# Optimization experiments

Measured on AMD Instinct MI355X. Metric: run time of the kernel, lower is better.

## Reference

```python
import jax, jax.numpy as jnp
import numpy as np
from jax import lax

B, N, C = 8, 8192, 91          # batch, num_boxes, num_classes (incl. background)
CM = C - 1                      # foreground classes
K = 1000                        # pre_nms_num_detections (per-class candidates / max per class)
MAX_TOTAL = 100                 # post_nms_num_detections
IOU_THR = 0.3
SCORE_THR = 0.0
BBOX_W = (10.0, 10.0, 5.0, 5.0)
BBOX_CLIP = float(np.log(1000.0 / 16.0))
IMG = 1024.0


def setup_inputs() -> dict:
    key = jax.random.key(0)
    k1, k2, k3, k4, k5, k6 = jax.random.split(key, 6)
    class_outputs = jax.random.normal(k1, (B, N, C), jnp.float32)
    box_outputs = jax.random.normal(k2, (B, N, C * 4), jnp.float32)
    cy = jax.random.uniform(k3, (B, N), minval=0.0, maxval=IMG)
    cx = jax.random.uniform(k4, (B, N), minval=0.0, maxval=IMG)
    sh = jax.random.uniform(k5, (B, N), minval=16.0, maxval=256.0)
    sw = jax.random.uniform(k6, (B, N), minval=16.0, maxval=256.0)
    anchor_boxes = jnp.stack([
        jnp.clip(cy - 0.5 * sh, 0.0, IMG), jnp.clip(cx - 0.5 * sw, 0.0, IMG),
        jnp.clip(cy + 0.5 * sh, 0.0, IMG), jnp.clip(cx + 0.5 * sw, 0.0, IMG)], axis=-1)
    image_info = jnp.tile(jnp.array([IMG, IMG, 1.0, 1.0], jnp.float32), (B, 1))
    return {"class_outputs": class_outputs, "box_outputs": box_outputs,
            "anchor_boxes": anchor_boxes, "image_info": image_info}


def decode_boxes(enc, anchors):
    # enc, anchors: [..., 4] (ty,tx,th,tw) / (ymin,xmin,ymax,xmax)
    wy, wx, wh, ww = BBOX_W
    ah = anchors[..., 2] - anchors[..., 0]
    aw = anchors[..., 3] - anchors[..., 1]
    acy = anchors[..., 0] + 0.5 * ah
    acx = anchors[..., 1] + 0.5 * aw
    ty = enc[..., 0] / wy
    tx = enc[..., 1] / wx
    th = jnp.minimum(enc[..., 2] / wh, BBOX_CLIP)
    tw = jnp.minimum(enc[..., 3] / ww, BBOX_CLIP)
    cy = ty * ah + acy
    cx = tx * aw + acx
    h = jnp.exp(th) * ah
    w = jnp.exp(tw) * aw
    return jnp.stack([cy - 0.5 * h, cx - 0.5 * w, cy + 0.5 * h, cx + 0.5 * w], axis=-1)


def pairwise_iou(b):  # b: [K,4] -> [K,K]
    area = jnp.maximum(b[:, 2] - b[:, 0], 0.0) * jnp.maximum(b[:, 3] - b[:, 1], 0.0)
    ih = jnp.maximum(jnp.minimum(b[:, None, 2], b[None, :, 2]) - jnp.maximum(b[:, None, 0], b[None, :, 0]), 0.0)
    iw = jnp.maximum(jnp.minimum(b[:, None, 3], b[None, :, 3]) - jnp.maximum(b[:, None, 1], b[None, :, 1]), 0.0)
    inter = ih * iw
    return inter / (area[:, None] + area[None, :] - inter + 1e-8)


def _per_class_nms(bc, sc):
    # bc: [N,4] normalized boxes, sc: [N] scores -> (kept boxes [K,4], scores [K], suppressed -> -1)
    sk, idx = lax.top_k(sc, K)
    bk = bc[idx]
    overlap = pairwise_iou(bk) > IOU_THR   # bool [K,K], sorted by score desc
    pass_thr = sk > SCORE_THR
    def body(i, keep):
        sup = jnp.any(keep & overlap[:, i])
        return keep.at[i].set(pass_thr[i] & jnp.logical_not(sup))
    keep = lax.fori_loop(0, K, body, jnp.zeros((K,), jnp.bool_))
    return bk, jnp.where(keep, sk, -1.0)


def _per_image(norm_boxes, sc):
    # norm_boxes: [N,CM,4], sc: [N,CM]
    bks, sks = jax.vmap(_per_class_nms)(jnp.transpose(norm_boxes, (1, 0, 2)), sc.T)
    fs = sks.reshape(-1)          # [CM*K]
    fb = bks.reshape(-1, 4)
    ts, ti = lax.top_k(fs, MAX_TOTAL)
    tb = fb[ti]
    tc = (ti // K).astype(jnp.float32)   # 0-based fg class index
    valid = ts > SCORE_THR
    ts = jnp.where(valid, ts, 0.0)
    tb = jnp.where(valid[:, None], tb, 0.0)
    tc = jnp.where(valid, tc, 0.0)
    return tb, ts, tc, jnp.sum(valid).astype(jnp.int32)


def reference(class_outputs, box_outputs, anchor_boxes, image_info):
    probs = jax.nn.softmax(class_outputs, axis=-1)
    scores = probs[..., 1:]                                   # [B,N,CM]
    enc = box_outputs.reshape(B, N, C, 4)[:, :, 1:, :]        # [B,N,CM,4]
    anchors = jnp.broadcast_to(anchor_boxes[:, :, None, :], (B, N, CM, 4))
    boxes = decode_boxes(enc, anchors)                        # [B,N,CM,4]
    h = image_info[:, 0]
    w = image_info[:, 1]
    hw = jnp.stack([h, w, h, w], axis=-1)                     # [B,4]
    boxes = jnp.clip(boxes, 0.0, hw[:, None, None, :])        # clip to image
    norm_boxes = boxes / hw[:, None, None, :]                 # to_normalized_coordinates
    pb, ps, pc, nv = lax.map(lambda a: _per_image(*a), (norm_boxes, scores))
    post_boxes = pb * hw[:, None, :]                          # to_absolute_coordinates
    post_classes = pc + 1.0                                   # shift back over background
    return (nv, post_boxes, post_classes, ps)
```

## Files before the change

### kernel.cpp

```cpp
#include <hip/hip_runtime.h>
#include <math.h>

#define Bb 8
#define Nn 8192
#define Cc 91
#define CM 90
#define Kk 1000
#define MAXT 100
#define KSEL 256
#define NW 4
#define IOU_THR 0.3f
#define BBOX_CLIP 4.135166556742356f
#define IMG 1024.0f
#define SM_ROWS 64

typedef unsigned long long u64;
typedef unsigned int u32;

__global__ __launch_bounds__(64) void softmax_scores(
    const float* __restrict__ cls, float* __restrict__ scores_t) {
    __shared__ float rowbuf[SM_ROWS * Cc];
    int blk = blockIdx.x;
    int lane = threadIdx.x;
    const float4* src = (const float4*)(cls + (size_t)blk * SM_ROWS * Cc);
    for (int i = lane; i < SM_ROWS * Cc / 4; i += 64) {
        float4 v = src[i];
        *(float4*)&rowbuf[i * 4] = v;
    }
    __syncthreads();
    int row_g = blk * SM_ROWS + lane;
    int b = row_g >> 13;
    int n = row_g & (Nn - 1);
    const float* row = &rowbuf[lane * Cc];
    float m = row[0];
    for (int c = 1; c < Cc; c++) m = fmaxf(m, row[c]);
    float s = 0.0f;
    for (int c = 0; c < Cc; c++) s += expf(row[c] - m);
    for (int c = 1; c < Cc; c++) {
        float p = expf(row[c] - m) / s;
        scores_t[((size_t)(b * CM + (c - 1))) * Nn + n] = p;
    }
}

__global__ __launch_bounds__(512) void topk_nms(
    const float* __restrict__ scores_t,
    const float* __restrict__ box_out, const float* __restrict__ anchors,
    u64* __restrict__ cand_key, float* __restrict__ cand_box) {
    __shared__ __align__(16) char smem[36896];
    u32* sbits = (u32*)smem;
    int* hist  = (int*)(smem + 32768);
    int* scal  = (int*)(smem + 36864);
    u64* keys  = (u64*)(smem + 32768);
    int* eqidx = (int*)(smem + 34816);
    u64* keys2 = (u64*)(smem);
    float* dy1 = (float*)(smem + 2048);
    float* dx1 = (float*)(smem + 3072);
    float* dy2 = (float*)(smem + 4096);
    float* dx2 = (float*)(smem + 5120);
    float* dar = (float*)(smem + 6144);
    float4* kb = (float4*)(smem + 7168);
    float* kar = (float*)(smem + 8768);
    u64* kkey  = (u64*)(smem + 9168);
    #define sh_need  scal[0]
    #define sh_digit scal[1]
    #define sh_cnt   scal[2]
    #define sh_eq    scal[3]
    #define sh_kcnt  scal[4]

    int bc = blockIdx.x;
    int b = bc / CM;
    int c = bc % CM;
    int tid = threadIdx.x;
    int wave = tid >> 6, lane = tid & 63;

    hist[tid] = 0;
    hist[tid + 512] = 0;
    if (tid == 0) { sh_need = KSEL; sh_cnt = 0; sh_eq = 0; }
    __syncthreads();

    const float4* s4 = (const float4*)(scores_t + (size_t)bc * Nn);
    float4 v0 = s4[tid];
    float4 v1 = s4[tid + 512];
    float4 v2 = s4[tid + 1024];
    float4 v3 = s4[tid + 1536];
    u32 x[16];
    x[0]  = __float_as_uint(v0.x); x[1]  = __float_as_uint(v0.y);
    x[2]  = __float_as_uint(v0.z); x[3]  = __float_as_uint(v0.w);
    x[4]  = __float_as_uint(v1.x); x[5]  = __float_as_uint(v1.y);
    x[6]  = __float_as_uint(v1.z); x[7]  = __float_as_uint(v1.w);
    x[8]  = __float_as_uint(v2.x); x[9]  = __float_as_uint(v2.y);
    x[10] = __float_as_uint(v2.z); x[11] = __float_as_uint(v2.w);
    x[12] = __float_as_uint(v3.x); x[13] = __float_as_uint(v3.y);
    x[14] = __float_as_uint(v3.z); x[15] = __float_as_uint(v3.w);
    *(uint4*)&sbits[(tid)        * 4] = make_uint4(x[0], x[1], x[2], x[3]);
    *(uint4*)&sbits[(tid + 512)  * 4] = make_uint4(x[4], x[5], x[6], x[7]);
    *(uint4*)&sbits[(tid + 1024) * 4] = make_uint4(x[8], x[9], x[10], x[11]);
    *(uint4*)&sbits[(tid + 1536) * 4] = make_uint4(x[12], x[13], x[14], x[15]);
    #pragma unroll
    for (int k = 0; k < 16; k++) atomicAdd(&hist[x[k] >> 20], 1);
    __syncthreads();

    #define SELECT_DIGIT()                                                   \
    if (wave == 0) {                                                         \
        int4 h0 = *(const int4*)&hist[16 * lane];                            \
        int4 h1 = *(const int4*)&hist[16 * lane + 4];                        \
        int4 h2 = *(const int4*)&hist[16 * lane + 8];                        \
        int4 h3 = *(const int4*)&hist[16 * lane + 12];                       \
        int cnt[16] = {h0.x, h0.y, h0.z, h0.w, h1.x, h1.y, h1.z, h1.w,       \
                       h2.x, h2.y, h2.z, h2.w, h3.x, h3.y, h3.z, h3.w};      \
        int gsum = 0;                                                        \
        _Pragma("unroll")                                                    \
        for (int j = 0; j < 16; j++) gsum += cnt[j];                         \
        int run = gsum;                                                      \
        for (int off = 1; off < 64; off <<= 1) {                             \
            int vv = __shfl_down(run, off, 64);                              \
            if (lane + off < 64) run += vv;                                  \
        }                                                                    \
        int sa = run - gsum;                                                 \
        int need = sh_need;                                                  \
        if (need > sa && need <= sa + gsum) {                                \
            int acc = sa;                                                    \
            _Pragma("unroll")                                                \
            for (int j = 15; j >= 0; j--) {                                  \
                if (acc + cnt[j] >= need) {                                  \
                    sh_digit = 16 * lane + j;                                \
                    sh_need = need - acc;                                    \
                    break;                                                   \
                }                                                            \
                acc += cnt[j];                                               \
            }                                                                \
        }                                                                    \
    }

    SELECT_DIGIT();
    __syncthreads();
    u32 P12 = (u32)sh_digit;

    hist[tid] = 0;
    hist[tid + 512] = 0;
    __syncthreads();
    for (int i = tid; i < Nn / 4; i += 512) {
        uint4 v = *(const uint4*)&sbits[i * 4];
        if ((v.x >> 20) == P12) atomicAdd(&hist[(v.x >> 10) & 1023], 1);
        if ((v.y >> 20) == P12) atomicAdd(&hist[(v.y >> 10) & 1023], 1);
        if ((v.z >> 20) == P12) atomicAdd(&hist[(v.z >> 10) & 1023], 1);
        if ((v.w >> 20) == P12) atomicAdd(&hist[(v.w >> 10) & 1023], 1);
    }
    __syncthreads();
    SELECT_DIGIT();
    __syncthreads();
    u32 P22 = (P12 << 10) | (u32)sh_digit;

    hist[tid] = 0;
    hist[tid + 512] = 0;
    __syncthreads();
    for (int i = tid; i < Nn / 4; i += 512) {
        uint4 v = *(const uint4*)&sbits[i * 4];
        if ((v.x >> 10) == P22) atomicAdd(&hist[v.x & 1023], 1);
        if ((v.y >> 10) == P22) atomicAdd(&hist[v.y & 1023], 1);
        if ((v.z >> 10) == P22) atomicAdd(&hist[v.z & 1023], 1);
        if ((v.w >> 10) == P22) atomicAdd(&hist[v.w & 1023], 1);
    }
    __syncthreads();
    SELECT_DIGIT();
    __syncthreads();
    u32 Tb = (P22 << 10) | (u32)sh_digit;
    int m = sh_need;
    #undef SELECT_DIGIT

    for (int i = tid; i < Nn / 4; i += 512) {
        uint4 v4 = *(const uint4*)&sbits[i * 4];
        u32 vs[4] = {v4.x, v4.y, v4.z, v4.w};
        #pragma unroll
        for (int k = 0; k < 4; k++) {
            u32 v = vs[k];
            int idx = i * 4 + k;
            if (v > Tb) {
                int pp = atomicAdd(&sh_cnt, 1);
                keys[pp] = ((u64)v << 13) | (u64)(8191 - idx);
            } else if (v == Tb) {
                int pp = atomicAdd(&sh_eq, 1);
                if (pp < 256) eqidx[pp] = idx;
            }
        }
    }
    __syncthreads();
    if (tid == 0) {
        int e = min(sh_eq, 256);
        for (int t = 0; t < m; t++) {
            int best = -1, bi = 0x7FFFFFFF;
            for (int q = 0; q < e; q++) {
                int ii = eqidx[q];
                if (ii < bi) { bi = ii; best = q; }
            }
            if (best >= 0) {
                eqidx[best] = 0x7FFFFFFF;
                int pp = atomicAdd(&sh_cnt, 1);
                keys[pp] = ((u64)Tb << 13) | (u64)(8191 - bi);
            }
        }
    }
    __syncthreads();

    if (tid < KSEL) {
        u64 my = keys[tid];
        int n = 8191 - (int)(my & 0x1FFF);
        const float4 e = *(const float4*)(box_out + ((size_t)(b * Nn + n)) * (Cc * 4) + (size_t)(c + 1) * 4);
        const float4 a = *(const float4*)(anchors + (size_t)(b * Nn + n) * 4);
        int r = 0;
        #pragma unroll 8
        for (int q = 0; q < KSEL; q++) r += (keys[q] > my) ? 1 : 0;
        keys2[r] = my;
        float ah = a.z - a.x, aw = a.w - a.y;
        float acy = a.x + 0.5f * ah, acx = a.y + 0.5f * aw;
        float ty = e.x / 10.0f, tx = e.y / 10.0f;
        float th = fminf(e.z / 5.0f, BBOX_CLIP);
        float tw = fminf(e.w / 5.0f, BBOX_CLIP);
        float cy = ty * ah + acy, cx = tx * aw + acx;
        float h = expf(th) * ah, w = expf(tw) * aw;
        float y1 = cy - 0.5f * h, x1 = cx - 0.5f * w;
        float y2 = cy + 0.5f * h, x2 = cx + 0.5f * w;
        y1 = fminf(fmaxf(y1, 0.0f), IMG) * (1.0f / IMG);
        x1 = fminf(fmaxf(x1, 0.0f), IMG) * (1.0f / IMG);
        y2 = fminf(fmaxf(y2, 0.0f), IMG) * (1.0f / IMG);
        x2 = fminf(fmaxf(x2, 0.0f), IMG) * (1.0f / IMG);
        float area = fmaxf(y2 - y1, 0.0f) * fmaxf(x2 - x1, 0.0f);
        dy1[r] = y1; dx1[r] = x1;
        dy2[r] = y2; dx2[r] = x2;
        dar[r] = area;
    }
    __syncthreads();

    if (tid < 64) {
        int kcnt = 0;
        for (int ci = 0; ci < NW && kcnt < MAXT; ci++) {
            int i = ci * 64 + lane;
            u64 key = keys2[i];
            float sc = __uint_as_float((u32)(key >> 13));
            float y1 = dy1[i], x1 = dx1[i];
            float y2 = dy2[i], x2 = dx2[i];
            float area = dar[i];

            bool sup = false;
            for (int r = 0; r < kcnt; r++) {
                float4 kv = kb[r];
                float ka = kar[r];
                float ih = fmaxf(fminf(kv.z, y2) - fmaxf(kv.x, y1), 0.0f);
                float iw = fmaxf(fminf(kv.w, x2) - fmaxf(kv.y, x1), 0.0f);
                float inter = ih * iw;
                sup = sup | (inter > IOU_THR * (ka + area - inter + 1e-8f));
            }
            u64 rem = __ballot((sc > 0.0f) && !sup);
            while (rem != 0ull && kcnt < MAXT) {
                int j = __ffsll(rem) - 1;
                rem &= rem - 1;
                float jy1 = __shfl(y1, j), jx1 = __shfl(x1, j);
                float jy2 = __shfl(y2, j), jx2 = __shfl(x2, j);
                float jar = __shfl(area, j);
                if (lane == j) {
                    kb[kcnt] = make_float4(y1, x1, y2, x2);
                    kar[kcnt] = area;
                    int flat = c * Kk + i;
                    kkey[kcnt] = ((u64)__float_as_uint(sc) << 32)
                               | ((u64)(u32)(131071 - flat) << 14)
                               | (u64)(u32)(c * MAXT + kcnt);
                }
                float ih = fmaxf(fminf(jy2, y2) - fmaxf(jy1, y1), 0.0f);
                float iw = fmaxf(fminf(jx2, x2) - fmaxf(jx1, x1), 0.0f);
                float inter = ih * iw;
                bool ov = inter > IOU_THR * (jar + area - inter + 1e-8f);
                u64 mm = __ballot(ov);
                rem &= ~mm;
                kcnt++;
            }
        }
        if (lane == 0) sh_kcnt = kcnt;
    }
    __syncthreads();

    int kcnt = sh_kcnt;
    for (int r = tid; r < MAXT; r += 512) {
        int slot = bc * MAXT + r;
        if (r < kcnt) {
            cand_key[slot] = kkey[r];
            float4 v = kb[r];
            cand_box[slot * 4 + 0] = v.x;
            cand_box[slot * 4 + 1] = v.y;
            cand_box[slot * 4 + 2] = v.z;
            cand_box[slot * 4 + 3] = v.w;
        } else {
            cand_key[slot] = 0ull;
        }
    }
    #undef sh_need
    #undef sh_digit
    #undef sh_cnt
    #undef sh_eq
    #undef sh_kcnt
}

__global__ __launch_bounds__(256) void final_topk(
    const u64* __restrict__ cand_key, const float* __restrict__ cand_box,
    float* __restrict__ out) {
    extern __shared__ u64 sk[];
    __shared__ u64 res[MAXT];
    int b = blockIdx.x;
    int tid = threadIdx.x;

    for (int i = tid; i < CM * MAXT; i += 256)
        sk[i] = cand_key[b * CM * MAXT + i];
    __syncthreads();

    if (tid < 64) {
        int lane = tid;
        int c0 = lane, c1 = lane + 64;
        bool h1 = c1 < CM;
        int p0 = 0, p1 = 0;
        u64 k0 = sk[c0 * MAXT + 0];
        u64 k0n = sk[c0 * MAXT + 1];
        u64 k1 = h1 ? sk[c1 * MAXT + 0] : 0ull;
        u64 k1n = h1 ? sk[c1 * MAXT + 1] : 0ull;
        for (int t = 0; t < MAXT; t++) {
            u64 m = (k0 > k1) ? k0 : k1;
            for (int off = 32; off > 0; off >>= 1) {
                u64 o = __shfl_xor(m, off);
                if (o > m) m = o;
            }
            if (lane == 0) res[t] = m;
            if (m != 0ull) {
                if (m == k0) {
                    p0++; k0 = k0n;
                    k0n = (p0 + 1 < MAXT) ? sk[c0 * MAXT + p0 + 1] : 0ull;
                } else if (h1 && m == k1) {
                    p1++; k1 = k1n;
                    k1n = (p1 + 1 < MAXT) ? sk[c1 * MAXT + p1 + 1] : 0ull;
                }
            }
        }
    }
    __syncthreads();

    for (int t = tid; t < MAXT; t += 256) {
        u64 m = res[t];
        float sc = __uint_as_float((u32)(m >> 32));
        bool valid = sc > 0.0f;
        float b0 = 0.f, b1 = 0.f, b2 = 0.f, b3 = 0.f, clsv = 0.f, sv = 0.f;
        if (valid) {
            int idx = (int)(m & 0x3FFF);
            int slot = b * CM * MAXT + idx;
            b0 = cand_box[slot * 4 + 0] * IMG;
            b1 = cand_box[slot * 4 + 1] * IMG;
            b2 = cand_box[slot * 4 + 2] * IMG;
            b3 = cand_box[slot * 4 + 3] * IMG;
            clsv = (float)(idx / MAXT + 1);
            sv = sc;
        }
        int o = (b * MAXT + t);
        out[8 + o * 4 + 0] = b0;
        out[8 + o * 4 + 1] = b1;
        out[8 + o * 4 + 2] = b2;
        out[8 + o * 4 + 3] = b3;
        out[8 + Bb * MAXT * 4 + o] = clsv;
        out[8 + Bb * MAXT * 5 + o] = sv;
    }
    if (tid == 0) {
        int nv = 0;
        for (int t = 0; t < MAXT; t++) nv += ((res[t] >> 32) != 0ull) ? 1 : 0;
        out[b] = (float)nv;
    }
}

extern "C" void kernel_launch(void* const* d_in, const int* in_sizes, int n_in,
                              void* d_out, int out_size, void* d_ws, size_t ws_size,
                              hipStream_t stream) {
    (void)in_sizes; (void)n_in; (void)out_size; (void)ws_size;
    const float* cls  = (const float*)d_in[0];
    const float* boxo = (const float*)d_in[1];
    const float* anch = (const float*)d_in[2];
    float* out = (float*)d_out;
    char* ws = (char*)d_ws;

    float* scores_t = (float*)(ws);
    u64*   cand_key = (u64*)  (ws + 23592960);
    float* cand_box = (float*)(ws + 24168960);

    softmax_scores<<<(Bb * Nn) / SM_ROWS, 64, 0, stream>>>(cls, scores_t);
    topk_nms<<<Bb * CM, 512, 0, stream>>>(scores_t, boxo, anch, cand_key, cand_box);
    final_topk<<<Bb, 256, CM * MAXT * sizeof(u64), stream>>>(cand_key, cand_box, out);
}
```

Baseline: 252.5 us.

## Split top-k selection and NMS into separate kernels; cache softmax exponentials

The fused top-k plus NMS kernel is split in two. A 512-thread selection kernel writes the 256 selected keys per class to workspace, and a 256-thread NMS/decode kernel with smaller shared memory reads them back. The aim is to let each phase run at a block size and occupancy suited to it, instead of holding 512 threads through the mostly serial NMS. The softmax kernel also stores each exponential in shared memory so expf is not computed twice. The cost is an extra kernel launch and a global round trip for the keys.

```diff
diff --git a/kernel.cpp b/kernel.cpp
--- a/kernel.cpp
+++ b/kernel.cpp
@@ -31,45 +31,36 @@
     int row_g = blk * SM_ROWS + lane;
     int b = row_g >> 13;
     int n = row_g & (Nn - 1);
-    const float* row = &rowbuf[lane * Cc];
+    float* row = &rowbuf[lane * Cc];
     float m = row[0];
     for (int c = 1; c < Cc; c++) m = fmaxf(m, row[c]);
     float s = 0.0f;
-    for (int c = 0; c < Cc; c++) s += expf(row[c] - m);
+    for (int c = 0; c < Cc; c++) {
+        float e = expf(row[c] - m);
+        row[c] = e;
+        s += e;
+    }
     for (int c = 1; c < Cc; c++) {
-        float p = expf(row[c] - m) / s;
+        float p = row[c] / s;
         scores_t[((size_t)(b * CM + (c - 1))) * Nn + n] = p;
     }
 }
 
-__global__ __launch_bounds__(512) void topk_nms(
+__global__ __launch_bounds__(512) void topk_select(
     const float* __restrict__ scores_t,
-    const float* __restrict__ box_out, const float* __restrict__ anchors,
-    u64* __restrict__ cand_key, float* __restrict__ cand_box) {
+    u64* __restrict__ keys_out) {
     __shared__ __align__(16) char smem[36896];
     u32* sbits = (u32*)smem;
     int* hist  = (int*)(smem + 32768);
     int* scal  = (int*)(smem + 36864);
     u64* keys  = (u64*)(smem + 32768);
     int* eqidx = (int*)(smem + 34816);
-    u64* keys2 = (u64*)(smem);
-    float* dy1 = (float*)(smem + 2048);
-    float* dx1 = (float*)(smem + 3072);
-    float* dy2 = (float*)(smem + 4096);
-    float* dx2 = (float*)(smem + 5120);
-    float* dar = (float*)(smem + 6144);
-    float4* kb = (float4*)(smem + 7168);
-    float* kar = (float*)(smem + 8768);
-    u64* kkey  = (u64*)(smem + 9168);
     #define sh_need  scal[0]
     #define sh_digit scal[1]
     #define sh_cnt   scal[2]
     #define sh_eq    scal[3]
-    #define sh_kcnt  scal[4]
 
     int bc = blockIdx.x;
-    int b = bc / CM;
-    int c = bc % CM;
     int tid = threadIdx.x;
     int wave = tid >> 6, lane = tid & 63;
 
@@ -202,6 +193,40 @@
     }
     __syncthreads();
 
+    if (tid < KSEL) keys_out[(size_t)bc * KSEL + tid] = keys[tid];
+    #undef sh_need
+    #undef sh_digit
+    #undef sh_cnt
+    #undef sh_eq
+}
+
+__global__ __launch_bounds__(256) void nms_decode(
+    const u64* __restrict__ keys_in,
+    const float* __restrict__ box_out, const float* __restrict__ anchors,
+    u64* __restrict__ cand_key, float* __restrict__ cand_box) {
+    __shared__ __align__(16) char smem[12928];
+    u64* keys  = (u64*)smem;
+    u64* keys2 = (u64*)(smem + 2048);
+    float* dy1 = (float*)(smem + 4096);
+    float* dx1 = (float*)(smem + 5120);
+    float* dy2 = (float*)(smem + 6144);
+    float* dx2 = (float*)(smem + 7168);
+    float* dar = (float*)(smem + 8192);
+    float4* kb = (float4*)(smem + 9216);
+    float* kar = (float*)(smem + 10816);
+    u64* kkey  = (u64*)(smem + 11216);
+    int* scal  = (int*)(smem + 12016);
+    #define sh_kcnt scal[0]
+
+    int bc = blockIdx.x;
+    int b = bc / CM;
+    int c = bc % CM;
+    int tid = threadIdx.x;
+    int lane = tid & 63;
+
+    if (tid < KSEL) keys[tid] = keys_in[(size_t)bc * KSEL + tid];
+    __syncthreads();
+
     if (tid < KSEL) {
         u64 my = keys[tid];
         int n = 8191 - (int)(my & 0x1FFF);
@@ -279,7 +304,7 @@
     __syncthreads();
 
     int kcnt = sh_kcnt;
-    for (int r = tid; r < MAXT; r += 512) {
+    for (int r = tid; r < MAXT; r += 256) {
         int slot = bc * MAXT + r;
         if (r < kcnt) {
             cand_key[slot] = kkey[r];
@@ -292,10 +317,6 @@
             cand_key[slot] = 0ull;
         }
     }
-    #undef sh_need
-    #undef sh_digit
-    #undef sh_cnt
-    #undef sh_eq
     #undef sh_kcnt
 }
 
@@ -383,8 +404,10 @@
     float* scores_t = (float*)(ws);
     u64*   cand_key = (u64*)  (ws + 23592960);
     float* cand_box = (float*)(ws + 24168960);
+    u64*   keys_ws  = (u64*)  (ws + 25320960);
 
     softmax_scores<<<(Bb * Nn) / SM_ROWS, 64, 0, stream>>>(cls, scores_t);
-    topk_nms<<<Bb * CM, 512, 0, stream>>>(scores_t, boxo, anch, cand_key, cand_box);
+    topk_select<<<Bb * CM, 512, 0, stream>>>(scores_t, keys_ws);
+    nms_decode<<<Bb * CM, 256, 0, stream>>>(keys_ws, boxo, anch, cand_key, cand_box);
     final_topk<<<Bb, 256, CM * MAXT * sizeof(u64), stream>>>(cand_key, cand_box, out);
 }
```

Result: no change. 253.7 us (+0.5%).

## Keep scores in registers for radix select; double-buffer histograms; cache softmax exps

Applied to the files above, without the earlier changes.

The top-k radix select no longer stages the 8192 scores in shared memory. Each thread keeps its 16 values in registers and re-scans them for every histogram pass and for the final compaction. Two histogram buffers alternate so one can be cleared while wave 0 selects a digit from the other, which removes separate clear-and-sync phases. Shared memory shrinks from about 36KB to 21KB, which may raise occupancy. Softmax also stores exp values in the shared row buffer instead of recomputing expf in the output loop.

```diff
diff --git a/kernel.cpp b/kernel.cpp
--- a/kernel.cpp
+++ b/kernel.cpp
@@ -31,13 +31,17 @@
     int row_g = blk * SM_ROWS + lane;
     int b = row_g >> 13;
     int n = row_g & (Nn - 1);
-    const float* row = &rowbuf[lane * Cc];
+    float* row = &rowbuf[lane * Cc];
     float m = row[0];
     for (int c = 1; c < Cc; c++) m = fmaxf(m, row[c]);
     float s = 0.0f;
-    for (int c = 0; c < Cc; c++) s += expf(row[c] - m);
+    for (int c = 0; c < Cc; c++) {
+        float e = expf(row[c] - m);
+        row[c] = e;
+        s += e;
+    }
     for (int c = 1; c < Cc; c++) {
-        float p = expf(row[c] - m) / s;
+        float p = row[c] / s;
         scores_t[((size_t)(b * CM + (c - 1))) * Nn + n] = p;
     }
 }
@@ -46,21 +50,21 @@
     const float* __restrict__ scores_t,
     const float* __restrict__ box_out, const float* __restrict__ anchors,
     u64* __restrict__ cand_key, float* __restrict__ cand_box) {
-    __shared__ __align__(16) char smem[36896];
-    u32* sbits = (u32*)smem;
-    int* hist  = (int*)(smem + 32768);
-    int* scal  = (int*)(smem + 36864);
-    u64* keys  = (u64*)(smem + 32768);
-    int* eqidx = (int*)(smem + 34816);
-    u64* keys2 = (u64*)(smem);
-    float* dy1 = (float*)(smem + 2048);
-    float* dx1 = (float*)(smem + 3072);
-    float* dy2 = (float*)(smem + 4096);
-    float* dx2 = (float*)(smem + 5120);
-    float* dar = (float*)(smem + 6144);
-    float4* kb = (float4*)(smem + 7168);
-    float* kar = (float*)(smem + 8768);
-    u64* kkey  = (u64*)(smem + 9168);
+    __shared__ __align__(16) char smem[21264];
+    int* hist1 = (int*)smem;
+    int* hist2 = (int*)(smem + 4096);
+    u64* keys  = (u64*)(smem + 8192);
+    int* eqidx = (int*)(smem + 10240);
+    u64* keys2 = (u64*)(smem + 11264);
+    float* dy1 = (float*)(smem + 13312);
+    float* dx1 = (float*)(smem + 14336);
+    float* dy2 = (float*)(smem + 15360);
+    float* dx2 = (float*)(smem + 16384);
+    float* dar = (float*)(smem + 17408);
+    float4* kb = (float4*)(smem + 18432);
+    float* kar = (float*)(smem + 20032);
+    u64* kkey  = (u64*)(smem + 20432);
+    int* scal  = (int*)(smem + 21232);
     #define sh_need  scal[0]
     #define sh_digit scal[1]
     #define sh_cnt   scal[2]
@@ -73,8 +77,8 @@
     int tid = threadIdx.x;
     int wave = tid >> 6, lane = tid & 63;
 
-    hist[tid] = 0;
-    hist[tid + 512] = 0;
+    hist1[tid] = 0; hist1[tid + 512] = 0;
+    hist2[tid] = 0; hist2[tid + 512] = 0;
     if (tid == 0) { sh_need = KSEL; sh_cnt = 0; sh_eq = 0; }
     __syncthreads();
 
@@ -92,20 +96,16 @@
     x[10] = __float_as_uint(v2.z); x[11] = __float_as_uint(v2.w);
     x[12] = __float_as_uint(v3.x); x[13] = __float_as_uint(v3.y);
     x[14] = __float_as_uint(v3.z); x[15] = __float_as_uint(v3.w);
-    *(uint4*)&sbits[(tid)        * 4] = make_uint4(x[0], x[1], x[2], x[3]);
-    *(uint4*)&sbits[(tid + 512)  * 4] = make_uint4(x[4], x[5], x[6], x[7]);
-    *(uint4*)&sbits[(tid + 1024) * 4] = make_uint4(x[8], x[9], x[10], x[11]);
-    *(uint4*)&sbits[(tid + 1536) * 4] = make_uint4(x[12], x[13], x[14], x[15]);
     #pragma unroll
-    for (int k = 0; k < 16; k++) atomicAdd(&hist[x[k] >> 20], 1);
-    __syncthreads();
-
-    #define SELECT_DIGIT()                                                   \
-    if (wave == 0) {                                                         \
-        int4 h0 = *(const int4*)&hist[16 * lane];                            \
-        int4 h1 = *(const int4*)&hist[16 * lane + 4];                        \
-        int4 h2 = *(const int4*)&hist[16 * lane + 8];                        \
-        int4 h3 = *(const int4*)&hist[16 * lane + 12];                       \
+    for (int k = 0; k < 16; k++) atomicAdd(&hist1[x[k] >> 20], 1);
+    __syncthreads();
+
+    #define SELECT_DIGIT(H)                                                  \
+    {                                                                        \
+        int4 h0 = *(const int4*)&(H)[16 * lane];                             \
+        int4 h1 = *(const int4*)&(H)[16 * lane + 4];                         \
+        int4 h2 = *(const int4*)&(H)[16 * lane + 8];                         \
+        int4 h3 = *(const int4*)&(H)[16 * lane + 12];                        \
         int cnt[16] = {h0.x, h0.y, h0.z, h0.w, h1.x, h1.y, h1.z, h1.w,       \
                        h2.x, h2.y, h2.z, h2.w, h3.x, h3.y, h3.z, h3.w};      \
         int gsum = 0;                                                        \
@@ -132,56 +132,41 @@
         }                                                                    \
     }
 
-    SELECT_DIGIT();
+    if (wave == 0) SELECT_DIGIT(hist1);
     __syncthreads();
     u32 P12 = (u32)sh_digit;
 
-    hist[tid] = 0;
-    hist[tid + 512] = 0;
-    __syncthreads();
-    for (int i = tid; i < Nn / 4; i += 512) {
-        uint4 v = *(const uint4*)&sbits[i * 4];
-        if ((v.x >> 20) == P12) atomicAdd(&hist[(v.x >> 10) & 1023], 1);
-        if ((v.y >> 20) == P12) atomicAdd(&hist[(v.y >> 10) & 1023], 1);
-        if ((v.z >> 20) == P12) atomicAdd(&hist[(v.z >> 10) & 1023], 1);
-        if ((v.w >> 20) == P12) atomicAdd(&hist[(v.w >> 10) & 1023], 1);
-    }
-    __syncthreads();
-    SELECT_DIGIT();
+    #pragma unroll
+    for (int k = 0; k < 16; k++)
+        if ((x[k] >> 20) == P12) atomicAdd(&hist2[(x[k] >> 10) & 1023], 1);
+    __syncthreads();
+
+    if (wave == 0) { SELECT_DIGIT(hist2); }
+    else { for (int i = tid - 64; i < 1024; i += 448) hist1[i] = 0; }
     __syncthreads();
     u32 P22 = (P12 << 10) | (u32)sh_digit;
 
-    hist[tid] = 0;
-    hist[tid + 512] = 0;
-    __syncthreads();
-    for (int i = tid; i < Nn / 4; i += 512) {
-        uint4 v = *(const uint4*)&sbits[i * 4];
-        if ((v.x >> 10) == P22) atomicAdd(&hist[v.x & 1023], 1);
-        if ((v.y >> 10) == P22) atomicAdd(&hist[v.y & 1023], 1);
-        if ((v.z >> 10) == P22) atomicAdd(&hist[v.z & 1023], 1);
-        if ((v.w >> 10) == P22) atomicAdd(&hist[v.w & 1023], 1);
-    }
-    __syncthreads();
-    SELECT_DIGIT();
+    #pragma unroll
+    for (int k = 0; k < 16; k++)
+        if ((x[k] >> 10) == P22) atomicAdd(&hist1[x[k] & 1023], 1);
+    __syncthreads();
+
+    if (wave == 0) SELECT_DIGIT(hist1);
     __syncthreads();
     u32 Tb = (P22 << 10) | (u32)sh_digit;
     int m = sh_need;
     #undef SELECT_DIGIT
 
-    for (int i = tid; i < Nn / 4; i += 512) {
-        uint4 v4 = *(const uint4*)&sbits[i * 4];
-        u32 vs[4] = {v4.x, v4.y, v4.z, v4.w};
-        #pragma unroll
-        for (int k = 0; k < 4; k++) {
-            u32 v = vs[k];
-            int idx = i * 4 + k;
-            if (v > Tb) {
-                int pp = atomicAdd(&sh_cnt, 1);
-                keys[pp] = ((u64)v << 13) | (u64)(8191 - idx);
-            } else if (v == Tb) {
-                int pp = atomicAdd(&sh_eq, 1);
-                if (pp < 256) eqidx[pp] = idx;
-            }
+    #pragma unroll
+    for (int k = 0; k < 16; k++) {
+        u32 v = x[k];
+        int idx = ((k >> 2) << 11) + (tid << 2) + (k & 3);
+        if (v > Tb) {
+            int pp = atomicAdd(&sh_cnt, 1);
+            keys[pp] = ((u64)v << 13) | (u64)(8191 - idx);
+        } else if (v == Tb) {
+            int pp = atomicAdd(&sh_eq, 1);
+            if (pp < 256) eqidx[pp] = idx;
         }
     }
     __syncthreads();
```

New measurement: 251.9 us. No clear change (-0.2%).
